# Performance work log

Measured on AMD Instinct MI355X. Metric: run time of the kernel, lower is better.

Reference implementation:

```python
import jax, jax.numpy as jnp
import numpy as np

B, M, N = 256, 256, 256

def setup_inputs() -> dict:
    key = jax.random.key(0)
    k1, k2 = jax.random.split(key)
    x_real = jax.random.normal(k1, (B, M, N), dtype=jnp.float32)
    x_imag = jax.random.normal(k2, (B, M, N), dtype=jnp.float32)
    return {"x_real": x_real, "x_imag": x_imag}

def reference(x_real, x_imag):
    # complex k-space input; original used complex128 via numpy on host,
    # we use complex64 (the natural accelerator precision), same math.
    x = jax.lax.complex(x_real, x_imag)  # [B, M, N]
    axes = (-2, -1)
    # centered 2D IFFT per sample (ifft_along_dim): fftshift(ifft2(ifftshift(x)))
    y = jnp.fft.fftshift(jnp.fft.ifft2(jnp.fft.ifftshift(x, axes=axes), axes=axes), axes=axes)
    y = y.reshape(-1, 1, M, N)  # (-1, 1, M, N) as in call()
    return (jnp.real(y), jnp.imag(y))
```

## Files before the change

kernel.cpp:

```cpp
#include <hip/hip_runtime.h>
#include <hip/hip_fp16.h>

namespace {

constexpr int NN   = 256;
constexpr int BMN  = 256 * 256 * 256;
constexpr int LPAD = 272;

typedef float f4 __attribute__((ext_vector_type(4)));

struct cpx { float re, im; };

__device__ __forceinline__ cpx cadd(cpx a, cpx b){ return cpx{a.re + b.re, a.im + b.im}; }
__device__ __forceinline__ cpx csub(cpx a, cpx b){ return cpx{a.re - b.re, a.im - b.im}; }
__device__ __forceinline__ cpx cmul(cpx a, cpx b){ return cpx{a.re*b.re - a.im*b.im, a.re*b.im + a.im*b.re}; }
__device__ __forceinline__ cpx cmuli(cpx a){ return cpx{-a.im, a.re}; }

__device__ __forceinline__ void r4(cpx a, cpx b, cpx c, cpx d,
                                   cpx& y0, cpx& y1, cpx& y2, cpx& y3) {
  cpx apc = cadd(a, c), amc = csub(a, c);
  cpx bpd = cadd(b, d), bmd = csub(b, d);
  cpx ib  = cmuli(bmd);
  y0 = cadd(apc, bpd);
  y1 = cadd(amc, ib);
  y2 = csub(apc, bpd);
  y3 = csub(amc, ib);
}

__device__ __forceinline__ void ifft16(cpx x[16]) {
  constexpr float WC[10] = { 1.f,  0.9238795325112867f,  0.7071067811865476f,  0.3826834323650898f, 0.f,
                            -0.3826834323650898f, -0.7071067811865476f, -0.9238795325112867f, -1.f,
                            -0.9238795325112867f };
  constexpr float WS[10] = { 0.f,  0.3826834323650898f,  0.7071067811865476f,  0.9238795325112867f, 1.f,
                             0.9238795325112867f,  0.7071067811865476f,  0.3826834323650898f,  0.f,
                            -0.3826834323650898f };
  cpx B[4][4];
#pragma unroll
  for (int n1 = 0; n1 < 4; ++n1)
    r4(x[n1], x[n1 + 4], x[n1 + 8], x[n1 + 12],
       B[n1][0], B[n1][1], B[n1][2], B[n1][3]);
#pragma unroll
  for (int n1 = 1; n1 < 4; ++n1)
#pragma unroll
    for (int k2 = 1; k2 < 4; ++k2)
      B[n1][k2] = cmul(B[n1][k2], cpx{WC[n1 * k2], WS[n1 * k2]});
#pragma unroll
  for (int k2 = 0; k2 < 4; ++k2)
    r4(B[0][k2], B[1][k2], B[2][k2], B[3][k2],
       x[k2], x[k2 + 4], x[k2 + 8], x[k2 + 12]);
}

__device__ __forceinline__ void twiddle256(cpx a[16], int t) {
  const float base = 0.024543692606170259f * (float)t;
#pragma unroll
  for (int k1 = 1; k1 < 16; ++k1) {
    float s, c;
    __sincosf(base * (float)k1, &s, &c);
    a[k1] = cmul(a[k1], cpx{c, s});
  }
}

__global__ __launch_bounds__(256)
void k_ifft_rows(const float* __restrict__ xr, const float* __restrict__ xi,
                 __half* __restrict__ wr, __half* __restrict__ wi) {
  __shared__ float Lr[16 * LPAD];
  __shared__ float Li[16 * LPAD];
  const int tid = threadIdx.x;
  const int t   = tid & 15;
  const int ll  = tid >> 4;

  const size_t blk = (size_t)blockIdx.x * (16 * NN);
  const f4* sr4 = reinterpret_cast<const f4*>(xr + blk);
  const f4* si4 = reinterpret_cast<const f4*>(xi + blk);

#pragma unroll
  for (int q = 0; q < 4; ++q) {
    const int fi   = (q << 8) + tid;
    const int line = fi >> 6;
    const int slot = fi & 63;
    const f4 vr = __builtin_nontemporal_load(&sr4[fi]);
    const f4 vi = __builtin_nontemporal_load(&si4[fi]);
    *reinterpret_cast<f4*>(&Lr[line * LPAD + slot * 4]) = vr;
    *reinterpret_cast<f4*>(&Li[line * LPAD + slot * 4]) = vi;
  }
  __syncthreads();

  cpx a[16];
  {
    const float* lr = Lr + ll * LPAD;
    const float* li = Li + ll * LPAD;
#pragma unroll
    for (int j = 0; j < 16; ++j) {
      const int idx = (((j << 4) | t) ^ 128);
      a[j] = cpx{ lr[idx], li[idx] };
    }
  }
  ifft16(a);
  twiddle256(a, t);
  __syncthreads();

  {
    float* lr = Lr + ll * LPAD;
    float* li = Li + ll * LPAD;
#pragma unroll
    for (int k1 = 0; k1 < 16; ++k1) { lr[k1 * 17 + t] = a[k1].re; li[k1 * 17 + t] = a[k1].im; }
    __syncthreads();
#pragma unroll
    for (int n2 = 0; n2 < 16; ++n2) { a[n2].re = lr[t * 17 + n2]; a[n2].im = li[t * 17 + n2]; }
  }
  ifft16(a);
  __syncthreads();

  {
    float* lr = Lr + ll * LPAD;
    float* li = Li + ll * LPAD;
#pragma unroll
    for (int k = 0; k < 16; ++k) {
      const int idx = (((k << 4) | t) ^ 128);
      lr[idx] = a[k].re;
      li[idx] = a[k].im;
    }
  }
  __syncthreads();

  constexpr float s1 = 1.0f / 256.0f;
  uint2* dr = reinterpret_cast<uint2*>(wr) + (size_t)blockIdx.x * 1024;
  uint2* di = reinterpret_cast<uint2*>(wi) + (size_t)blockIdx.x * 1024;
#pragma unroll
  for (int q = 0; q < 4; ++q) {
    const int fi   = (q << 8) + tid;
    const int line = fi >> 6;
    const int slot = fi & 63;
    const f4 vr = *reinterpret_cast<const f4*>(&Lr[line * LPAD + slot * 4]);
    const f4 vi = *reinterpret_cast<const f4*>(&Li[line * LPAD + slot * 4]);
    union { __half2 h[2]; uint2 u; } pr, pi_;
    pr.h[0]  = __floats2half2_rn(vr.x * s1, vr.y * s1);
    pr.h[1]  = __floats2half2_rn(vr.z * s1, vr.w * s1);
    pi_.h[0] = __floats2half2_rn(vi.x * s1, vi.y * s1);
    pi_.h[1] = __floats2half2_rn(vi.z * s1, vi.w * s1);
    dr[fi] = pr.u;
    di[fi] = pi_.u;
  }
}

__global__ __launch_bounds__(512)
void k_ifft_cols(const __half* __restrict__ wr, const __half* __restrict__ wi,
                 float* __restrict__ yr, float* __restrict__ yi) {
  __shared__ float lbuf[32 * 273];
  const int tid = threadIdx.x;
  const int c   = tid & 31;
  const int t   = tid >> 5;
  const int b   = blockIdx.x >> 3;
  const int c0  = (blockIdx.x & 7) << 5;
  const int base = b * 65536 + c0 + c;

  cpx a[16];
#pragma unroll
  for (int j = 0; j < 16; ++j) {
    const int m = (((j << 4) | t) ^ 128);
    a[j] = cpx{ __half2float(wr[base + m * NN]), __half2float(wi[base + m * NN]) };
  }
  ifft16(a);
  twiddle256(a, t);

  {
    float* L = lbuf + c * 273;
#pragma unroll
    for (int k1 = 0; k1 < 16; ++k1) L[k1 * 17 + t] = a[k1].re;
    __syncthreads();
    float br[16];
#pragma unroll
    for (int n2 = 0; n2 < 16; ++n2) br[n2] = L[t * 17 + n2];
    __syncthreads();
#pragma unroll
    for (int k1 = 0; k1 < 16; ++k1) L[k1 * 17 + t] = a[k1].im;
    __syncthreads();
#pragma unroll
    for (int n2 = 0; n2 < 16; ++n2) { a[n2].im = L[t * 17 + n2]; a[n2].re = br[n2]; }
  }

  ifft16(a);
  constexpr float sc = 1.0f / 256.0f;
#pragma unroll
  for (int k = 0; k < 16; ++k) {
    const int m = (((k << 4) | t) ^ 128);
    __builtin_nontemporal_store(a[k].re * sc, &yr[base + m * NN]);
    __builtin_nontemporal_store(a[k].im * sc, &yi[base + m * NN]);
  }
}

}

extern "C" void kernel_launch(void* const* d_in, const int* in_sizes, int n_in,
                              void* d_out, int out_size, void* d_ws, size_t ws_size,
                              hipStream_t stream) {
  const float* xr = (const float*)d_in[0];
  const float* xi = (const float*)d_in[1];
  float* yr = (float*)d_out;
  float* yi = yr + BMN;
  __half* wr = (__half*)d_ws;
  __half* wi = wr + BMN;

  k_ifft_rows<<<4096, 256, 0, stream>>>(xr, xi, wr, wi);
  k_ifft_cols<<<2048, 512, 0, stream>>>(wr, wi, yr, yi);
}
```

Measured before the change: 82.64 us.

## Loop row kernel over four tiles with register prefetch of next tile

The row-FFT kernel now handles four 16-row tiles per block, launching a quarter as many blocks. While the current tile is transformed, the next tile's global loads are issued into registers so memory latency overlaps compute. Nontemporal loads become ordinary loads. The cost is more registers per thread and fewer blocks to spread across CUs (1024 blocks on 256 CUs).

```diff
diff --git a/kernel.cpp b/kernel.cpp
--- a/kernel.cpp
+++ b/kernel.cpp
@@ -3,9 +3,10 @@
 
 namespace {
 
-constexpr int NN   = 256;
-constexpr int BMN  = 256 * 256 * 256;
-constexpr int LPAD = 272;
+constexpr int NN    = 256;
+constexpr int BMN   = 256 * 256 * 256;
+constexpr int LPAD  = 272;
+constexpr int TILES = 4;
 
 typedef float f4 __attribute__((ext_vector_type(4)));
 
@@ -69,77 +70,102 @@
   const int t   = tid & 15;
   const int ll  = tid >> 4;
 
-  const size_t blk = (size_t)blockIdx.x * (16 * NN);
-  const f4* sr4 = reinterpret_cast<const f4*>(xr + blk);
-  const f4* si4 = reinterpret_cast<const f4*>(xi + blk);
-
-#pragma unroll
-  for (int q = 0; q < 4; ++q) {
-    const int fi   = (q << 8) + tid;
-    const int line = fi >> 6;
-    const int slot = fi & 63;
-    const f4 vr = __builtin_nontemporal_load(&sr4[fi]);
-    const f4 vi = __builtin_nontemporal_load(&si4[fi]);
-    *reinterpret_cast<f4*>(&Lr[line * LPAD + slot * 4]) = vr;
-    *reinterpret_cast<f4*>(&Li[line * LPAD + slot * 4]) = vi;
-  }
-  __syncthreads();
-
-  cpx a[16];
+  const size_t base0 = (size_t)blockIdx.x * (TILES * 16 * NN);
+
+  f4 pr[4], pim[4];
   {
-    const float* lr = Lr + ll * LPAD;
-    const float* li = Li + ll * LPAD;
-#pragma unroll
-    for (int j = 0; j < 16; ++j) {
-      const int idx = (((j << 4) | t) ^ 128);
-      a[j] = cpx{ lr[idx], li[idx] };
-    }
-  }
-  ifft16(a);
-  twiddle256(a, t);
-  __syncthreads();
-
-  {
-    float* lr = Lr + ll * LPAD;
-    float* li = Li + ll * LPAD;
-#pragma unroll
-    for (int k1 = 0; k1 < 16; ++k1) { lr[k1 * 17 + t] = a[k1].re; li[k1 * 17 + t] = a[k1].im; }
-    __syncthreads();
-#pragma unroll
-    for (int n2 = 0; n2 < 16; ++n2) { a[n2].re = lr[t * 17 + n2]; a[n2].im = li[t * 17 + n2]; }
-  }
-  ifft16(a);
-  __syncthreads();
-
-  {
-    float* lr = Lr + ll * LPAD;
-    float* li = Li + ll * LPAD;
-#pragma unroll
-    for (int k = 0; k < 16; ++k) {
-      const int idx = (((k << 4) | t) ^ 128);
-      lr[idx] = a[k].re;
-      li[idx] = a[k].im;
-    }
-  }
-  __syncthreads();
-
-  constexpr float s1 = 1.0f / 256.0f;
-  uint2* dr = reinterpret_cast<uint2*>(wr) + (size_t)blockIdx.x * 1024;
-  uint2* di = reinterpret_cast<uint2*>(wi) + (size_t)blockIdx.x * 1024;
-#pragma unroll
-  for (int q = 0; q < 4; ++q) {
-    const int fi   = (q << 8) + tid;
-    const int line = fi >> 6;
-    const int slot = fi & 63;
-    const f4 vr = *reinterpret_cast<const f4*>(&Lr[line * LPAD + slot * 4]);
-    const f4 vi = *reinterpret_cast<const f4*>(&Li[line * LPAD + slot * 4]);
-    union { __half2 h[2]; uint2 u; } pr, pi_;
-    pr.h[0]  = __floats2half2_rn(vr.x * s1, vr.y * s1);
-    pr.h[1]  = __floats2half2_rn(vr.z * s1, vr.w * s1);
-    pi_.h[0] = __floats2half2_rn(vi.x * s1, vi.y * s1);
-    pi_.h[1] = __floats2half2_rn(vi.z * s1, vi.w * s1);
-    dr[fi] = pr.u;
-    di[fi] = pi_.u;
+    const f4* sr4 = reinterpret_cast<const f4*>(xr + base0);
+    const f4* si4 = reinterpret_cast<const f4*>(xi + base0);
+#pragma unroll
+    for (int q = 0; q < 4; ++q) {
+      const int fi = (q << 8) + tid;
+      pr[q]  = sr4[fi];
+      pim[q] = si4[fi];
+    }
+  }
+
+  for (int it = 0; it < TILES; ++it) {
+    const size_t tileoff = base0 + (size_t)it * (16 * NN);
+    __syncthreads();
+
+#pragma unroll
+    for (int q = 0; q < 4; ++q) {
+      const int fi   = (q << 8) + tid;
+      const int line = fi >> 6;
+      const int slot = fi & 63;
+      *reinterpret_cast<f4*>(&Lr[line * LPAD + slot * 4]) = pr[q];
+      *reinterpret_cast<f4*>(&Li[line * LPAD + slot * 4]) = pim[q];
+    }
+    __syncthreads();
+
+    if (it + 1 < TILES) {
+      const size_t nb = tileoff + (16 * NN);
+      const f4* sr4 = reinterpret_cast<const f4*>(xr + nb);
+      const f4* si4 = reinterpret_cast<const f4*>(xi + nb);
+#pragma unroll
+      for (int q = 0; q < 4; ++q) {
+        const int fi = (q << 8) + tid;
+        pr[q]  = sr4[fi];
+        pim[q] = si4[fi];
+      }
+    }
+
+    cpx a[16];
+    {
+      const float* lr = Lr + ll * LPAD;
+      const float* li = Li + ll * LPAD;
+#pragma unroll
+      for (int j = 0; j < 16; ++j) {
+        const int idx = (((j << 4) | t) ^ 128);
+        a[j] = cpx{ lr[idx], li[idx] };
+      }
+    }
+    ifft16(a);
+    twiddle256(a, t);
+    __syncthreads();
+
+    {
+      float* lr = Lr + ll * LPAD;
+      float* li = Li + ll * LPAD;
+#pragma unroll
+      for (int k1 = 0; k1 < 16; ++k1) { lr[k1 * 17 + t] = a[k1].re; li[k1 * 17 + t] = a[k1].im; }
+      __syncthreads();
+#pragma unroll
+      for (int n2 = 0; n2 < 16; ++n2) { a[n2].re = lr[t * 17 + n2]; a[n2].im = li[t * 17 + n2]; }
+    }
+    ifft16(a);
+    __syncthreads();
+
+    {
+      float* lr = Lr + ll * LPAD;
+      float* li = Li + ll * LPAD;
+#pragma unroll
+      for (int k = 0; k < 16; ++k) {
+        const int idx = (((k << 4) | t) ^ 128);
+        lr[idx] = a[k].re;
+        li[idx] = a[k].im;
+      }
+    }
+    __syncthreads();
+
+    constexpr float s1 = 1.0f / 256.0f;
+    uint2* dr = reinterpret_cast<uint2*>(wr + tileoff);
+    uint2* di = reinterpret_cast<uint2*>(wi + tileoff);
+#pragma unroll
+    for (int q = 0; q < 4; ++q) {
+      const int fi   = (q << 8) + tid;
+      const int line = fi >> 6;
+      const int slot = fi & 63;
+      const f4 vr = *reinterpret_cast<const f4*>(&Lr[line * LPAD + slot * 4]);
+      const f4 vi = *reinterpret_cast<const f4*>(&Li[line * LPAD + slot * 4]);
+      union { __half2 h[2]; uint2 u; } hr, hi;
+      hr.h[0] = __floats2half2_rn(vr.x * s1, vr.y * s1);
+      hr.h[1] = __floats2half2_rn(vr.z * s1, vr.w * s1);
+      hi.h[0] = __floats2half2_rn(vi.x * s1, vi.y * s1);
+      hi.h[1] = __floats2half2_rn(vi.z * s1, vi.w * s1);
+      dr[fi] = hr.u;
+      di[fi] = hi.u;
+    }
   }
 }
 
@@ -201,6 +227,6 @@
   __half* wr = (__half*)d_ws;
   __half* wi = wr + BMN;
 
-  k_ifft_rows<<<4096, 256, 0, stream>>>(xr, xi, wr, wi);
+  k_ifft_rows<<<1024, 256, 0, stream>>>(xr, xi, wr, wi);
   k_ifft_cols<<<2048, 512, 0, stream>>>(wr, wi, yr, yi);
 }
```

New measurement: 80.78 us. 2.3% less time.
